# Kernel optimization log

Measured on AMD Instinct MI355X. Metric: run time of the kernel, lower is better.

## Reference

```python
import jax, jax.numpy as jnp
import numpy as np

B, N, F_IN = 512, 128, 133
NHID, NHEADS, HID = 64, 8, 512
FP_DIM, FP2, TASKS = 1489, 512, 12
ALPHA = 0.2
NEG_BIG = -9e15


def _lin_init(key, fan_in, fan_out):
    return jax.random.normal(key, (fan_in, fan_out), jnp.float32) / np.sqrt(fan_in)


def setup_inputs() -> dict:
    key = jax.random.key(0)
    ks = jax.random.split(key, 24)
    inp = {
        'h': jax.random.normal(ks[0], (B, N, F_IN), jnp.float32),
        'adj': jax.random.randint(ks[1], (B, N, N), 0, 2, jnp.int32),
        'edge_feat': jax.random.uniform(ks[2], (B, N, N), jnp.float32),
        'fp': jax.random.uniform(ks[3], (B, FP_DIM), jnp.float32),
        # multi-head GAT layer params (a split as [a1; a2; a_edge])
        'W_heads': jax.random.normal(ks[4], (NHEADS, F_IN, NHID), jnp.float32) / np.sqrt(F_IN),
        'a1_heads': jax.random.normal(ks[5], (NHEADS, NHID), jnp.float32) / np.sqrt(NHID),
        'a2_heads': jax.random.normal(ks[6], (NHEADS, NHID), jnp.float32) / np.sqrt(NHID),
        'ae_heads': jax.random.normal(ks[7], (NHEADS,), jnp.float32) * 0.1,
        # output GAT layer
        'W_out': jax.random.normal(ks[8], (NHID * NHEADS, HID), jnp.float32) / np.sqrt(NHID * NHEADS),
        'a1_out': jax.random.normal(ks[9], (HID,), jnp.float32) / np.sqrt(HID),
        'a2_out': jax.random.normal(ks[10], (HID,), jnp.float32) / np.sqrt(HID),
        'ae_out': jax.random.normal(ks[11], ()) * 0.1,
        # FPN
        'fc1_w': _lin_init(ks[12], FP_DIM, FP2), 'fc1_b': jnp.zeros((FP2,), jnp.float32),
        'fc2_w': _lin_init(ks[13], FP2, HID), 'fc2_b': jnp.zeros((HID,), jnp.float32),
        # cross-attention fusion
        'q_w': _lin_init(ks[14], HID, HID), 'q_b': jnp.zeros((HID,), jnp.float32),
        'k_w': _lin_init(ks[15], HID, HID), 'k_b': jnp.zeros((HID,), jnp.float32),
        'v_w': _lin_init(ks[16], HID, HID), 'v_b': jnp.zeros((HID,), jnp.float32),
        'o_w': _lin_init(ks[17], HID, HID), 'o_b': jnp.zeros((HID,), jnp.float32),
        # FFN head
        'ffn1_w': _lin_init(ks[18], HID, HID), 'ffn1_b': jnp.zeros((HID,), jnp.float32),
        'ffn2_w': _lin_init(ks[19], HID, TASKS), 'ffn2_b': jnp.zeros((TASKS,), jnp.float32),
    }
    return inp


def _leaky(x):
    return jnp.where(x >= 0, x, ALPHA * x)


def _fpgnn_forward(h, adj, edge_feat, fp,
                   W_heads, a1_heads, a2_heads, ae_heads,
                   W_out, a1_out, a2_out, ae_out,
                   fc1_w, fc1_b, fc2_w, fc2_b,
                   q_w, q_b, k_w, k_b, v_w, v_b, o_w, o_b,
                   ffn1_w, ffn1_b, ffn2_w, ffn2_b):
    mask = adj > 0  # [B,N,N]
    # --- multi-head GAT layers (concat=True) ---
    Wh = jnp.einsum('bnf,hfd->bhnd', h, W_heads)            # [B,H,N,D]
    s1 = jnp.einsum('bhnd,hd->bhn', Wh, a1_heads)
    s2 = jnp.einsum('bhnd,hd->bhn', Wh, a2_heads)
    # e[b,h,i,j] = leaky(Wh_i.a1 + Wh_j.a2 + edge_ij*ae)  (exact decomposition of
    # the original concat([Wh_i, Wh_j, edge_ij]) @ a)
    e = _leaky(s1[:, :, :, None] + s2[:, :, None, :]
               + edge_feat[:, None, :, :] * ae_heads[None, :, None, None])
    att = jnp.where(mask[:, None], e, NEG_BIG)
    att = jax.nn.softmax(att, axis=-1)                       # softmax over dim=1 of [N,N]
    hp = jnp.einsum('bhij,bhjd->bhid', att, Wh)
    x = jax.nn.elu(hp)                                       # concat=True -> ELU
    x = jnp.transpose(x, (0, 2, 1, 3)).reshape(B, N, NHEADS * NHID)
    # --- output GAT layer (concat=False) ---
    Wx = x @ W_out                                           # [B,N,HID]
    t1 = Wx @ a1_out                                         # [B,N]
    t2 = Wx @ a2_out
    e2 = _leaky(t1[:, :, None] + t2[:, None, :] + edge_feat * ae_out)
    att2 = jnp.where(mask, e2, NEG_BIG)
    att2 = jax.nn.softmax(att2, axis=-1)
    hp2 = jnp.einsum('bij,bjd->bid', att2, Wx)
    gat_nodes = jax.nn.elu(hp2)                              # F.elu in GATOne
    gat_out = gat_nodes.mean(axis=1)                         # molecule readout [B,HID]
    # --- FPN ---
    fpn_out = jax.nn.relu(fp @ fc1_w + fc1_b) @ fc2_w + fc2_b  # [B,HID]
    # --- cross-attention fusion ---
    q = gat_out @ q_w + q_b
    k = fpn_out @ k_w + k_b
    v = fpn_out @ v_w + v_b
    score = jnp.sum(q * k, axis=-1, keepdims=True) / np.sqrt(HID)  # [B,1]
    weight = jax.nn.softmax(score[:, :, None], axis=-1)[:, :, 0]    # softmax over size-1 dim -> ones
    fused = q + weight * v
    fused = jax.nn.relu(fused @ o_w + o_b)
    # --- FFN head (dropout p=0, eval) ---
    out = jax.nn.relu(fused @ ffn1_w + ffn1_b) @ ffn2_w + ffn2_b
    return out


def reference(h, adj, edge_feat, fp,
              W_heads, a1_heads, a2_heads, ae_heads,
              W_out, a1_out, a2_out, ae_out,
              fc1_w, fc1_b, fc2_w, fc2_b,
              q_w, q_b, k_w, k_b, v_w, v_b, o_w, o_b,
              ffn1_w, ffn1_b, ffn2_w, ffn2_b):
    return _fpgnn_forward(h, adj, edge_feat, fp,
                          W_heads, a1_heads, a2_heads, ae_heads,
                          W_out, a1_out, a2_out, ae_out,
                          fc1_w, fc1_b, fc2_w, fc2_b,
                          q_w, q_b, k_w, k_b, v_w, v_b, o_w, o_b,
                          ffn1_w, ffn1_b, ffn2_w, ffn2_b)
```

## Files before the change

kernel.cpp:

```cpp
#include <hip/hip_runtime.h>
#include <hip/hip_bf16.h>


#define ALPHA_LK 0.2f
#define LOG2E 1.44269504f
#define KP1 192
#define KPF 1536
#define MINF_BF16 0xFF80u

typedef unsigned short ushort_t;
typedef __attribute__((ext_vector_type(8))) short bfrag;
typedef __attribute__((ext_vector_type(4))) float ffrag;

__device__ __forceinline__ float b2f(ushort_t u) {
  return __uint_as_float(((unsigned)u) << 16);
}
__device__ __forceinline__ ushort_t f2b(float f) {
  unsigned u = __float_as_uint(f);
  unsigned r = (u + 0x7fffu + ((u >> 16) & 1u)) >> 16;
  return (ushort_t)r;
}
__device__ __forceinline__ unsigned cvt_pk(float lo, float hi) {
  unsigned r;
  asm("v_cvt_pk_bf16_f32 %0, %1, %2" : "=v"(r) : "v"(lo), "v"(hi));
  return r;
}
__device__ __forceinline__ float frcp(float x) {
  float r;
  asm("v_rcp_f32 %0, %1" : "=v"(r) : "v"(x));
  return r;
}
__device__ __forceinline__ float fexp2(float x) {
#if __has_builtin(__builtin_amdgcn_exp2f)
  return __builtin_amdgcn_exp2f(x);
#else
  return exp2f(x);
#endif
}
__device__ __forceinline__ float elu1(float v) {
  return v > 0.f ? v : __expf(v) - 1.f;
}

__device__ __forceinline__ void gll16(const void* g, void* l) {
  __builtin_amdgcn_global_load_lds(
      (const __attribute__((address_space(1))) unsigned int*)(unsigned long long)g,
      (__attribute__((address_space(3))) unsigned int*)(unsigned long long)l,
      16, 0, 0);
}

__global__ __launch_bounds__(256) void prep_all(
    const float* __restrict__ h, const int* __restrict__ adj,
    const float* __restrict__ edge, const float* __restrict__ fp,
    const float* __restrict__ Whd, const float* __restrict__ a1h,
    const float* __restrict__ a2h,
    const float* __restrict__ W_out, const float* __restrict__ a1o,
    const float* __restrict__ a2o,
    const float* __restrict__ fc1_w, const float* __restrict__ fc2_w,
    const float* __restrict__ q_w, const float* __restrict__ v_w,
    const float* __restrict__ o_w, const float* __restrict__ ffn1_w,
    const float* __restrict__ qb, const float* __restrict__ vb,
    ushort_t* __restrict__ hb, ushort_t* __restrict__ em,
    ushort_t* __restrict__ W2t, ushort_t* __restrict__ fpb,
    ushort_t* __restrict__ fc1t,
    ushort_t* __restrict__ Wot, ushort_t* __restrict__ fc2t,
    ushort_t* __restrict__ qwt, ushort_t* __restrict__ vwt,
    ushort_t* __restrict__ owt, ushort_t* __restrict__ f1t,
    float* __restrict__ wa1, float* __restrict__ wa2,
    ushort_t* __restrict__ wh12, float* __restrict__ qvb) {
  int bid = blockIdx.x;
  const int t = threadIdx.x;

  if (bid < 8) {
    int hh = bid;
    if (t < 192) {
      float s1 = 0.f, s2 = 0.f;
      if (t < 133) {
        const float* wr = Whd + (size_t)(hh * 133 + t) * 64;
        const float* a1r = a1h + hh * 64;
        const float* a2r = a2h + hh * 64;
#pragma unroll 8
        for (int d = 0; d < 64; ++d) {
          float wv = wr[d];
          s1 += wv * a1r[d];
          s2 += wv * a2r[d];
        }
      }
      wh12[hh * 384 + t] = f2b(s1);
      wh12[hh * 384 + 192 + t] = f2b(s2);
    }
    return;
  }
  bid -= 8;
  if (bid < 128) {
    int wv = t >> 6, lane = t & 63;
    int k = bid * 4 + wv;
    const float* wr = W_out + (size_t)k * 512;
    float p1 = 0.f, p2 = 0.f;
#pragma unroll
    for (int i = 0; i < 8; ++i) {
      float v = wr[lane + i * 64];
      p1 += v * a1o[lane + i * 64];
      p2 += v * a2o[lane + i * 64];
    }
#pragma unroll
    for (int off = 32; off; off >>= 1) {
      p1 += __shfl_down(p1, off);
      p2 += __shfl_down(p2, off);
    }
    if (lane == 0) { wa1[k] = p1; wa2[k] = p2; }
    return;
  }
  bid -= 128;
  if (bid < 2) {
    int o = bid * 256 + t;
    qvb[o] = qb[o] + vb[o];
    return;
  }
  bid -= 2;
  if (bid < 96) {
    int o = bid * 256 + t;
    if (o < 512 * 48) {
      int col = o / 48, c4 = (o - col * 48) * 4;
      int hh = col >> 6, d = col & 63;
      ushort4 v;
      v.x = (c4 + 0 < 133) ? f2b(Whd[(hh * 133 + c4 + 0) * 64 + d]) : (ushort_t)0;
      v.y = (c4 + 1 < 133) ? f2b(Whd[(hh * 133 + c4 + 1) * 64 + d]) : (ushort_t)0;
      v.z = (c4 + 2 < 133) ? f2b(Whd[(hh * 133 + c4 + 2) * 64 + d]) : (ushort_t)0;
      v.w = (c4 + 3 < 133) ? f2b(Whd[(hh * 133 + c4 + 3) * 64 + d]) : (ushort_t)0;
      *(ushort4*)&W2t[(size_t)col * KP1 + c4] = v;
    }
    return;
  }
  bid -= 96;
  if (bid < 768) {
    int o = bid * 256 + t;
    int row = o / 384, c4 = (o - row * 384) * 4;
    const float* fr = fp + (size_t)row * 1489;
    ushort4 v;
    v.x = (c4 + 0 < 1489) ? f2b(fr[c4 + 0]) : (ushort_t)0;
    v.y = (c4 + 1 < 1489) ? f2b(fr[c4 + 1]) : (ushort_t)0;
    v.z = (c4 + 2 < 1489) ? f2b(fr[c4 + 2]) : (ushort_t)0;
    v.w = (c4 + 3 < 1489) ? f2b(fr[c4 + 3]) : (ushort_t)0;
    *(ushort4*)&fpb[(size_t)row * KPF + c4] = v;
    return;
  }
  bid -= 768;
  if (bid < 768) {
    int o = bid * 256 + t;
    int col = o / 384, k4 = (o - col * 384) * 4;
    ushort4 v;
    v.x = (k4 + 0 < 1489) ? f2b(fc1_w[(size_t)(k4 + 0) * 512 + col]) : (ushort_t)0;
    v.y = (k4 + 1 < 1489) ? f2b(fc1_w[(size_t)(k4 + 1) * 512 + col]) : (ushort_t)0;
    v.z = (k4 + 2 < 1489) ? f2b(fc1_w[(size_t)(k4 + 2) * 512 + col]) : (ushort_t)0;
    v.w = (k4 + 3 < 1489) ? f2b(fc1_w[(size_t)(k4 + 3) * 512 + col]) : (ushort_t)0;
    *(ushort4*)&fc1t[(size_t)col * KPF + k4] = v;
    return;
  }
  bid -= 768;
  if (bid < 1536) {
    int y = bid >> 8;
    int o = (bid & 255) * 256 + t;
    const float* W = y == 0 ? W_out : y == 1 ? fc2_w : y == 2 ? q_w
                   : y == 3 ? v_w : y == 4 ? o_w : ffn1_w;
    ushort_t* Wt = y == 0 ? Wot : y == 1 ? fc2t : y == 2 ? qwt
                 : y == 3 ? vwt : y == 4 ? owt : f1t;
    int col = o >> 7, k4 = (o & 127) * 4;
    ushort4 v;
    v.x = f2b(W[(size_t)(k4 + 0) * 512 + col]);
    v.y = f2b(W[(size_t)(k4 + 1) * 512 + col]);
    v.z = f2b(W[(size_t)(k4 + 2) * 512 + col]);
    v.w = f2b(W[(size_t)(k4 + 3) * 512 + col]);
    *(ushort4*)&Wt[(size_t)col * 512 + k4] = v;
    return;
  }
  bid -= 1536;
  if (bid < 12288) {
    int o = bid * 256 + t;
    int row = o / 48, c4 = (o - row * 48) * 4;
    const float* hr = h + (size_t)row * 133;
    ushort4 v;
    v.x = (c4 + 0 < 133) ? f2b(hr[c4 + 0]) : (ushort_t)0;
    v.y = (c4 + 1 < 133) ? f2b(hr[c4 + 1]) : (ushort_t)0;
    v.z = (c4 + 2 < 133) ? f2b(hr[c4 + 2]) : (ushort_t)0;
    v.w = (c4 + 3 < 133) ? f2b(hr[c4 + 3]) : (ushort_t)0;
    *(ushort4*)&hb[(size_t)row * KP1 + c4] = v;
    return;
  }
  bid -= 12288;
  {
    size_t o = ((size_t)bid * 256 + t) * 4;
    float4 e = *(const float4*)&edge[o];
    int4 a = *(const int4*)&adj[o];
    ushort4 v;
    v.x = a.x > 0 ? f2b(e.x) : (ushort_t)MINF_BF16;
    v.y = a.y > 0 ? f2b(e.y) : (ushort_t)MINF_BF16;
    v.z = a.z > 0 ? f2b(e.z) : (ushort_t)MINF_BF16;
    v.w = a.w > 0 ? f2b(e.w) : (ushort_t)MINF_BF16;
    *(ushort4*)&em[o] = v;
  }
}

__global__ __launch_bounds__(256) void att2t(
    const ushort_t* __restrict__ xb, const ushort_t* __restrict__ em,
    const float* __restrict__ wa1, const float* __restrict__ wa2,
    const float* __restrict__ aeo,
    ushort_t* __restrict__ awg, float* __restrict__ sinvg, int base) {
  __shared__ float t1s[128], t2s[128];
  __shared__ float was1[512], was2[512];
  const int bl = blockIdx.x, bg = base + bl;
  const int t = threadIdx.x;
  was1[t] = wa1[t]; was1[t + 256] = wa1[t + 256];
  was2[t] = wa2[t]; was2[t + 256] = wa2[t + 256];
  __syncthreads();
  const int row = t >> 1, half = t & 1;
  {
    const ushort_t* xr = xb + (size_t)(bl * 128 + row) * 512 + half * 256;
    float p1 = 0.f, p2 = 0.f;
#pragma unroll 4
    for (int i = 0; i < 32; ++i) {
      uint4 u = *(const uint4*)&xr[i * 8];
      const unsigned uu[4] = {u.x, u.y, u.z, u.w};
#pragma unroll
      for (int pr = 0; pr < 4; ++pr) {
        float lo = __uint_as_float(uu[pr] << 16);
        float hi = __uint_as_float(uu[pr] & 0xffff0000u);
        int c = half * 256 + i * 8 + pr * 2;
        p1 = fmaf(lo, was1[c], p1); p1 = fmaf(hi, was1[c + 1], p1);
        p2 = fmaf(lo, was2[c], p2); p2 = fmaf(hi, was2[c + 1], p2);
      }
    }
    p1 += __shfl_xor(p1, 1);
    p2 += __shfl_xor(p2, 1);
    if (!half) { t1s[row] = p1 * LOG2E; t2s[row] = p2 * LOG2E; }
  }
  __syncthreads();
  const float ae2 = aeo[0] * LOG2E;
  const float rt1 = t1s[row];
  const ushort_t* emr = em + (size_t)bg * 16384 + row * 128 + half * 64;
  ushort_t* awr = awg + (size_t)bl * 16384 + row * 128 + half * 64;
  float s = 0.f;
#pragma unroll
  for (int v = 0; v < 8; ++v) {
    uint4 eu = *(const uint4*)&emr[v * 8];
    const unsigned uu[4] = {eu.x, eu.y, eu.z, eu.w};
    unsigned po[4];
#pragma unroll
    for (int pr = 0; pr < 4; ++pr) {
      float elo = __uint_as_float(uu[pr] << 16);
      float ehi = __uint_as_float(uu[pr] & 0xffff0000u);
      float e0 = fmaf(elo, ae2, rt1 + t2s[half * 64 + v * 8 + pr * 2]);
      float e1 = fmaf(ehi, ae2, rt1 + t2s[half * 64 + v * 8 + pr * 2 + 1]);
      e0 = fmaxf(e0, ALPHA_LK * e0);
      e1 = fmaxf(e1, ALPHA_LK * e1);
      float p0 = (elo != -INFINITY) ? fexp2(e0) : 0.f;
      float p1 = (ehi != -INFINITY) ? fexp2(e1) : 0.f;
      unsigned q = cvt_pk(p0, p1);
      po[pr] = q;
      s += __uint_as_float(q << 16) + __uint_as_float(q & 0xffff0000u);
    }
    *(uint4*)&awr[v * 8] = make_uint4(po[0], po[1], po[2], po[3]);
  }
  s += __shfl_xor(s, 1);
  if (!half) sinvg[(size_t)bl * 128 + row] = 1.f / fmaxf(s, 1e-30f);
}

__global__ __launch_bounds__(256) void fused_gat1(
    const ushort_t* __restrict__ hb, const ushort_t* __restrict__ W2t,
    const ushort_t* __restrict__ edgeM, const ushort_t* __restrict__ wh12g,
    const float* __restrict__ ae,
    ushort_t* __restrict__ x, int base) {
  __shared__ union {
    struct { ushort_t As[128][64]; ushort_t Bs[64][64]; } g;
    ushort_t WS[64][136];
  } u;
  __shared__ float ss1[128], ss2[128];
  __shared__ ushort_t wh12s[2][192];
  const int id = blockIdx.x;
  const int hh = (id >> 3) & 7;
  const int bl = ((id >> 6) << 3) | (id & 7);
  const int bg = base + bl;
  const int t = threadIdx.x;
  const int lane = t & 63, w = t >> 6;
  const int l16 = lane & 15, quad = lane >> 4;
  const int w8 = w * 8, sr8 = (t >> 3) & 7;
  const int csw = ((t & 7) ^ sr8) << 3;

  if (t < 96)
    *(ushort4*)&(&wh12s[0][0])[t * 4] =
        *(const ushort4*)&wh12g[hh * 384 + t * 4];

  const ushort_t* gA = hb + (size_t)(bl * 128 + w8 + sr8) * KP1 + csw;
  const ushort_t* gB = W2t + (size_t)(hh * 64 + w8 + sr8) * KP1 + csw;
  ffrag acc[2][4];
  ffrag acc_s[2];
#pragma unroll
  for (int mi = 0; mi < 2; ++mi) {
    acc_s[mi] = {0.f, 0.f, 0.f, 0.f};
#pragma unroll
    for (int ni = 0; ni < 4; ++ni) acc[mi][ni] = {0.f, 0.f, 0.f, 0.f};
  }
  for (int k0 = 0; k0 < KP1; k0 += 64) {
    __syncthreads();
#pragma unroll
    for (int p = 0; p < 4; ++p)
      gll16(gA + (size_t)(p * 32) * KP1 + k0, &u.g.As[p * 32 + w8][0]);
#pragma unroll
    for (int p = 0; p < 2; ++p)
      gll16(gB + (size_t)(p * 32) * KP1 + k0, &u.g.Bs[p * 32 + w8][0]);
    __syncthreads();
#pragma unroll
    for (int ks = 0; ks < 2; ++ks) {
      const int cs = ((ks * 4 + quad) ^ (l16 & 7)) << 3;
      bfrag af[2], bf[4];
      bfrag bs = {0, 0, 0, 0, 0, 0, 0, 0};
      if (l16 < 2)
        bs = *(const bfrag*)&wh12s[l16][k0 + ks * 32 + quad * 8];
#pragma unroll
      for (int mi = 0; mi < 2; ++mi)
        af[mi] = *(const bfrag*)&u.g.As[w * 32 + mi * 16 + l16][cs];
#pragma unroll
      for (int ni = 0; ni < 4; ++ni)
        bf[ni] = *(const bfrag*)&u.g.Bs[ni * 16 + l16][cs];
#pragma unroll
      for (int mi = 0; mi < 2; ++mi) {
#pragma unroll
        for (int ni = 0; ni < 4; ++ni)
          acc[mi][ni] = __builtin_amdgcn_mfma_f32_16x16x32_bf16(
              af[mi], bf[ni], acc[mi][ni], 0, 0, 0);
        acc_s[mi] = __builtin_amdgcn_mfma_f32_16x16x32_bf16(
            af[mi], bs, acc_s[mi], 0, 0, 0);
      }
    }
  }
  __syncthreads();

#pragma unroll
  for (int mi = 0; mi < 2; ++mi)
#pragma unroll
    for (int ni = 0; ni < 4; ++ni) {
      int col = ni * 16 + l16;
      int rowb = w * 32 + mi * 16 + quad * 4;
      uint2 pv;
      pv.x = cvt_pk(acc[mi][ni][0], acc[mi][ni][1]);
      pv.y = cvt_pk(acc[mi][ni][2], acc[mi][ni][3]);
      *(uint2*)&u.WS[col][rowb] = pv;
    }
  if (l16 < 2) {
    float* sp = (l16 == 0) ? ss1 : ss2;
#pragma unroll
    for (int mi = 0; mi < 2; ++mi)
#pragma unroll
      for (int r = 0; r < 4; ++r)
        sp[w * 32 + mi * 16 + quad * 4 + r] = acc_s[mi][r] * LOG2E;
  }
  uint4 ereg[2][4];
  {
    const ushort_t* em = edgeM + (size_t)bg * 16384;
#pragma unroll
    for (int mi = 0; mi < 2; ++mi) {
      int row = w * 32 + mi * 16 + l16;
#pragma unroll
      for (int ks = 0; ks < 4; ++ks)
        ereg[mi][ks] = *(const uint4*)&em[row * 128 + ks * 32 + quad * 8];
    }
  }
  __syncthreads();

  const float aeh2 = ae[hh] * LOG2E;
  float rs1[2];
  rs1[0] = ss1[w * 32 + l16];
  rs1[1] = ss1[w * 32 + 16 + l16];
  uint4 aw[2][4];
#pragma unroll
  for (int mi = 0; mi < 2; ++mi) {
#pragma unroll
    for (int ks = 0; ks < 4; ++ks) {
      float s2v[8];
      *(float4*)&s2v[0] = *(const float4*)&ss2[ks * 32 + quad * 8];
      *(float4*)&s2v[4] = *(const float4*)&ss2[ks * 32 + quad * 8 + 4];
      const unsigned uu[4] = {ereg[mi][ks].x, ereg[mi][ks].y,
                              ereg[mi][ks].z, ereg[mi][ks].w};
      unsigned po[4];
#pragma unroll
      for (int pr = 0; pr < 4; ++pr) {
        float elo = __uint_as_float(uu[pr] << 16);
        float ehi = __uint_as_float(uu[pr] & 0xffff0000u);
        float e0 = fmaf(elo, aeh2, rs1[mi] + s2v[pr * 2]);
        float e1 = fmaf(ehi, aeh2, rs1[mi] + s2v[pr * 2 + 1]);
        e0 = fmaxf(e0, ALPHA_LK * e0);
        e1 = fmaxf(e1, ALPHA_LK * e1);
        float p0 = (elo != -INFINITY) ? fexp2(e0) : 0.f;
        float p1 = (ehi != -INFINITY) ? fexp2(e1) : 0.f;
        po[pr] = cvt_pk(p0, p1);
      }
      aw[mi][ks] = make_uint4(po[0], po[1], po[2], po[3]);
    }
  }

  bfrag bones;
#pragma unroll
  for (int i = 0; i < 8; ++i) bones[i] = (short)0x3F80;

  ffrag acc2[2][4];
  ffrag accs[2];
#pragma unroll
  for (int mi = 0; mi < 2; ++mi) {
    accs[mi] = {0.f, 0.f, 0.f, 0.f};
#pragma unroll
    for (int ni = 0; ni < 4; ++ni) acc2[mi][ni] = {0.f, 0.f, 0.f, 0.f};
  }
#pragma unroll
  for (int ks = 0; ks < 4; ++ks) {
    bfrag bfr[4];
#pragma unroll
    for (int ni = 0; ni < 4; ++ni)
      bfr[ni] = *(const bfrag*)&u.WS[ni * 16 + l16][ks * 32 + quad * 8];
#pragma unroll
    for (int mi = 0; mi < 2; ++mi) {
      bfrag afr;
      __builtin_memcpy(&afr, &aw[mi][ks], 16);
#pragma unroll
      for (int ni = 0; ni < 4; ++ni)
        acc2[mi][ni] = __builtin_amdgcn_mfma_f32_16x16x32_bf16(
            afr, bfr[ni], acc2[mi][ni], 0, 0, 0);
      accs[mi] = __builtin_amdgcn_mfma_f32_16x16x32_bf16(
          afr, bones, accs[mi], 0, 0, 0);
    }
  }
  float sv[2][4];
#pragma unroll
  for (int mi = 0; mi < 2; ++mi)
#pragma unroll
    for (int r = 0; r < 4; ++r)
      sv[mi][r] = frcp(fmaxf(accs[mi][r], 1e-30f));

#pragma unroll
  for (int mi = 0; mi < 2; ++mi)
#pragma unroll
    for (int ni = 0; ni < 4; ++ni) {
      float e0 = elu1(acc2[mi][ni][0] * sv[mi][0]);
      float e1 = elu1(acc2[mi][ni][1] * sv[mi][1]);
      float e2 = elu1(acc2[mi][ni][2] * sv[mi][2]);
      float e3 = elu1(acc2[mi][ni][3] * sv[mi][3]);
      unsigned p01 = cvt_pk(e0, e1), p23 = cvt_pk(e2, e3);
      int rl = w * 32 + mi * 16 + quad * 4;
      size_t bo = (size_t)(bl * 128 + rl) * 512 + hh * 64 + ni * 16 + l16;
      x[bo] = (ushort_t)p01;
      x[bo + 512] = (ushort_t)(p01 >> 16);
      x[bo + 1024] = (ushort_t)p23;
      x[bo + 1536] = (ushort_t)(p23 >> 16);
    }
}

__global__ __launch_bounds__(256) void fused_gat2(
    const ushort_t* __restrict__ xb, const ushort_t* __restrict__ Wot,
    const ushort_t* __restrict__ awg, const float* __restrict__ sinvg,
    ushort_t* __restrict__ gatb, int base) {
  __shared__ union {
    struct { ushort_t As[128][64]; ushort_t Bs[128][64]; } g;
    ushort_t WS[128][136];
  } u;
  __shared__ float ps[4][64];
  const int id = blockIdx.x;
  const int sp2 = (id >> 3) & 3;
  const int bl = ((id >> 5) << 3) | (id & 7);
  const int bg = base + bl;
  const int t = threadIdx.x;
  const int lane = t & 63, w = t >> 6;
  const int wm = w >> 1, wn = w & 1;
  const int l16 = lane & 15, quad = lane >> 4;
  const int w8 = w * 8, sr8 = (t >> 3) & 7;
  const int csw = ((t & 7) ^ sr8) << 3;

  const ushort_t* gA = xb + (size_t)(bl * 128 + w8 + sr8) * 512 + csw;
  const ushort_t* gB = Wot + (size_t)(sp2 * 128 + w8 + sr8) * 512 + csw;
  ffrag acc[4][4];
#pragma unroll
  for (int mi = 0; mi < 4; ++mi)
#pragma unroll
    for (int ni = 0; ni < 4; ++ni) acc[mi][ni] = {0.f, 0.f, 0.f, 0.f};
  for (int k0 = 0; k0 < 512; k0 += 64) {
    __syncthreads();
#pragma unroll
    for (int p = 0; p < 4; ++p) {
      gll16(gA + (size_t)(p * 32) * 512 + k0, &u.g.As[p * 32 + w8][0]);
      gll16(gB + (size_t)(p * 32) * 512 + k0, &u.g.Bs[p * 32 + w8][0]);
    }
    __syncthreads();
#pragma unroll
    for (int ks = 0; ks < 2; ++ks) {
      const int cs = ((ks * 4 + quad) ^ (l16 & 7)) << 3;
      bfrag af[4], bf[4];
#pragma unroll
      for (int i = 0; i < 4; ++i) {
        af[i] = *(const bfrag*)&u.g.As[wm * 64 + i * 16 + l16][cs];
        bf[i] = *(const bfrag*)&u.g.Bs[wn * 64 + i * 16 + l16][cs];
      }
#pragma unroll
      for (int mi = 0; mi < 4; ++mi)
#pragma unroll
        for (int ni = 0; ni < 4; ++ni)
          acc[mi][ni] = __builtin_amdgcn_mfma_f32_16x16x32_bf16(
              af[mi], bf[ni], acc[mi][ni], 0, 0, 0);
    }
  }
  __syncthreads();

#pragma unroll
  for (int mi = 0; mi < 4; ++mi)
#pragma unroll
    for (int ni = 0; ni < 4; ++ni) {
      int col = wn * 64 + ni * 16 + l16;
      int rowb = wm * 64 + mi * 16 + quad * 4;
      uint2 pv;
      pv.x = cvt_pk(acc[mi][ni][0], acc[mi][ni][1]);
      pv.y = cvt_pk(acc[mi][ni][2], acc[mi][ni][3]);
      *(uint2*)&u.WS[col][rowb] = pv;
    }
  __syncthreads();

  uint4 awf[2][4];
  float sv[2][4];
  {
    const ushort_t* ap = awg + (size_t)bl * 16384;
#pragma unroll
    for (int mi = 0; mi < 2; ++mi) {
      int row = w * 32 + mi * 16 + l16;
#pragma unroll
      for (int ks = 0; ks < 4; ++ks)
        awf[mi][ks] = *(const uint4*)&ap[row * 128 + ks * 32 + quad * 8];
      float si = sinvg[(size_t)bl * 128 + row];
#pragma unroll
      for (int r = 0; r < 4; ++r) sv[mi][r] = __shfl(si, quad * 4 + r);
    }
  }

  for (int s0 = 0; s0 < 2; ++s0) {
    ffrag acc2[2][4];
#pragma unroll
    for (int mi = 0; mi < 2; ++mi)
#pragma unroll
      for (int ni = 0; ni < 4; ++ni) acc2[mi][ni] = {0.f, 0.f, 0.f, 0.f};
#pragma unroll
    for (int ks = 0; ks < 4; ++ks) {
      bfrag bfr[4];
#pragma unroll
      for (int ni = 0; ni < 4; ++ni)
        bfr[ni] = *(const bfrag*)&u.WS[s0 * 64 + ni * 16 + l16][ks * 32 + quad * 8];
#pragma unroll
      for (int mi = 0; mi < 2; ++mi) {
        bfrag afr;
        __builtin_memcpy(&afr, &awf[mi][ks], 16);
#pragma unroll
        for (int ni = 0; ni < 4; ++ni)
          acc2[mi][ni] = __builtin_amdgcn_mfma_f32_16x16x32_bf16(
              afr, bfr[ni], acc2[mi][ni], 0, 0, 0);
      }
    }
    __syncthreads();
#pragma unroll
    for (int ni = 0; ni < 4; ++ni) {
      float s = 0.f;
#pragma unroll
      for (int mi = 0; mi < 2; ++mi)
#pragma unroll
        for (int r = 0; r < 4; ++r) s += elu1(acc2[mi][ni][r] * sv[mi][r]);
      s += __shfl_xor(s, 16);
      s += __shfl_xor(s, 32);
      if (quad == 0) ps[w][ni * 16 + l16] = s;
    }
    __syncthreads();
    if (t < 64) {
      float s = ps[0][t] + ps[1][t] + ps[2][t] + ps[3][t];
      gatb[(size_t)bg * 512 + sp2 * 128 + s0 * 64 + t] = f2b(s * (1.f / 128.f));
    }
  }
}

__device__ __forceinline__ void tail_kloop(
    const ushort_t* __restrict__ A, const ushort_t* __restrict__ Bt,
    int K, int ld, ushort_t (*As)[64], ushort_t (*Bs)[64],
    ffrag (*acc)[4], int row0, int col0, int t) {
  const int lane = t & 63, w = t >> 6;
  const int wm = w >> 1, wn = w & 1;
  const int l16 = lane & 15, quad = lane >> 4;
  const int w8 = w * 8, sr8 = (t >> 3) & 7;
  const int csw = ((t & 7) ^ sr8) << 3;
  const ushort_t* gA = A + (size_t)(row0 + w8 + sr8) * ld + csw;
  const ushort_t* gB = Bt + (size_t)(col0 + w8 + sr8) * ld + csw;
  for (int k0 = 0; k0 < K; k0 += 64) {
    __syncthreads();
#pragma unroll
    for (int p = 0; p < 4; ++p) {
      gll16(gA + (size_t)(p * 32) * ld + k0, &As[p * 32 + w8][0]);
      gll16(gB + (size_t)(p * 32) * ld + k0, &Bs[p * 32 + w8][0]);
    }
    __syncthreads();
#pragma unroll
    for (int ks = 0; ks < 2; ++ks) {
      const int cs = ((ks * 4 + quad) ^ (l16 & 7)) << 3;
      bfrag af[4], bf[4];
#pragma unroll
      for (int i = 0; i < 4; ++i) {
        af[i] = *(const bfrag*)&As[wm * 64 + i * 16 + l16][cs];
        bf[i] = *(const bfrag*)&Bs[wn * 64 + i * 16 + l16][cs];
      }
#pragma unroll
      for (int mi = 0; mi < 4; ++mi)
#pragma unroll
        for (int ni = 0; ni < 4; ++ni)
          acc[mi][ni] = __builtin_amdgcn_mfma_f32_16x16x32_bf16(
              af[mi], bf[ni], acc[mi][ni], 0, 0, 0);
    }
  }
}

template <int DUAL, int RELU>
__global__ __launch_bounds__(256) void gemm_tail(
    const ushort_t* __restrict__ A1, const ushort_t* __restrict__ Bt1,
    int K1, int ld1,
    const ushort_t* __restrict__ A2, const ushort_t* __restrict__ Bt2,
    const float* __restrict__ bias, ushort_t* __restrict__ C) {
  __shared__ ushort_t As[128][64];
  __shared__ ushort_t Bs[128][64];
  const int t = threadIdx.x;
  const int lane = t & 63, w = t >> 6;
  const int wm = w >> 1, wn = w & 1;
  const int l16 = lane & 15, quad = lane >> 4;
  const int row0 = blockIdx.y * 128, col0 = blockIdx.x * 128;

  ffrag acc[4][4];
#pragma unroll
  for (int mi = 0; mi < 4; ++mi)
#pragma unroll
    for (int ni = 0; ni < 4; ++ni) acc[mi][ni] = {0.f, 0.f, 0.f, 0.f};

  tail_kloop(A1, Bt1, K1, ld1, As, Bs, acc, row0, col0, t);
  if (DUAL) tail_kloop(A2, Bt2, 512, 512, As, Bs, acc, row0, col0, t);

#pragma unroll
  for (int mi = 0; mi < 4; ++mi)
#pragma unroll
    for (int ni = 0; ni < 4; ++ni) {
      int col = col0 + wn * 64 + ni * 16 + l16;
      float bb = bias[col];
      float v0 = acc[mi][ni][0] + bb, v1 = acc[mi][ni][1] + bb;
      float v2 = acc[mi][ni][2] + bb, v3 = acc[mi][ni][3] + bb;
      if (RELU) {
        v0 = fmaxf(v0, 0.f); v1 = fmaxf(v1, 0.f);
        v2 = fmaxf(v2, 0.f); v3 = fmaxf(v3, 0.f);
      }
      unsigned p01 = cvt_pk(v0, v1), p23 = cvt_pk(v2, v3);
      int row = row0 + wm * 64 + mi * 16 + quad * 4;
      size_t o = (size_t)row * 512 + col;
      C[o] = (ushort_t)p01;
      C[o + 512] = (ushort_t)(p01 >> 16);
      C[o + 1024] = (ushort_t)p23;
      C[o + 1536] = (ushort_t)(p23 >> 16);
    }
}

__global__ __launch_bounds__(256) void ffn2_kernel(
    const ushort_t* __restrict__ f5, const float* __restrict__ W,
    const float* __restrict__ b, float* __restrict__ out) {
  int wv = threadIdx.x >> 6, lane = threadIdx.x & 63;
  int row = blockIdx.x * 4 + wv;
  const ushort_t* fr = f5 + (size_t)row * 512;
  float v[8];
  ushort4 u0 = *(const ushort4*)&fr[lane * 8];
  ushort4 u1 = *(const ushort4*)&fr[lane * 8 + 4];
  v[0] = b2f(u0.x); v[1] = b2f(u0.y); v[2] = b2f(u0.z); v[3] = b2f(u0.w);
  v[4] = b2f(u1.x); v[5] = b2f(u1.y); v[6] = b2f(u1.z); v[7] = b2f(u1.w);
#pragma unroll
  for (int j = 0; j < 12; ++j) {
    float s = 0.f;
#pragma unroll
    for (int i = 0; i < 8; ++i) s += v[i] * W[(size_t)(lane * 8 + i) * 12 + j];
#pragma unroll
    for (int off = 32; off; off >>= 1) s += __shfl_down(s, off);
    if (lane == 0) out[(size_t)row * 12 + j] = s + b[j];
  }
}

extern "C" void kernel_launch(void* const* d_in, const int* in_sizes, int n_in,
                              void* d_out, int out_size, void* d_ws, size_t ws_size,
                              hipStream_t stream) {
  const float* h        = (const float*)d_in[0];
  const int*   adj      = (const int*)d_in[1];
  const float* edge     = (const float*)d_in[2];
  const float* fp       = (const float*)d_in[3];
  const float* W_heads  = (const float*)d_in[4];
  const float* a1_heads = (const float*)d_in[5];
  const float* a2_heads = (const float*)d_in[6];
  const float* ae_heads = (const float*)d_in[7];
  const float* W_out  = (const float*)d_in[8];
  const float* a1_out = (const float*)d_in[9];
  const float* a2_out = (const float*)d_in[10];
  const float* ae_out = (const float*)d_in[11];
  const float* fc1_w = (const float*)d_in[12];
  const float* fc1_b = (const float*)d_in[13];
  const float* fc2_w = (const float*)d_in[14];
  const float* fc2_b = (const float*)d_in[15];
  const float* q_w = (const float*)d_in[16];
  const float* q_b = (const float*)d_in[17];
  const float* v_w = (const float*)d_in[20];
  const float* v_b = (const float*)d_in[21];
  const float* o_w = (const float*)d_in[22];
  const float* o_b = (const float*)d_in[23];
  const float* ffn1_w = (const float*)d_in[24];
  const float* ffn1_b = (const float*)d_in[25];
  const float* ffn2_w = (const float*)d_in[26];
  const float* ffn2_b = (const float*)d_in[27];
  float* out = (float*)d_out;

  const size_t hb_bytes = (size_t)65536 * KP1 * 2;
  const size_t em_bytes = (size_t)512 * 16384 * 2;
  const size_t tail_bytes =
      (size_t)512 * KPF * 2 * 2 + (size_t)512 * 512 * 2 * 12 + 2048;
  const size_t fixed_bytes = hb_bytes + em_bytes + (size_t)512 * KP1 * 2 +
                             (size_t)2 * 65536 * 4 + tail_bytes + 16384;
  int C = 32;
  for (int cand = 512; cand >= 32; cand >>= 1) {
    size_t need = (size_t)cand * (131072 + 32768 + 512) + fixed_bytes;
    if (need <= ws_size) { C = cand; break; }
  }
  const int M = C * 128;
  (void)M;

  char* p = (char*)d_ws;
  ushort_t* xb  = (ushort_t*)p; p += (size_t)C * 65536 * 2;
  ushort_t* awg = (ushort_t*)p; p += (size_t)C * 16384 * 2;
  float* sinv   = (float*)p;    p += (size_t)C * 128 * 4;
  ushort_t* hb  = (ushort_t*)p; p += hb_bytes;
  ushort_t* em  = (ushort_t*)p; p += em_bytes;
  ushort_t* W2t = (ushort_t*)p; p += (size_t)512 * KP1 * 2;
  ushort_t* wh12 = (ushort_t*)p; p += 8 * 384 * 2;
  float* t_unused = (float*)p; p += 2 * 65536 * 4 - 8 * 384 * 2;
  (void)t_unused;
  ushort_t* fpb  = (ushort_t*)p; p += (size_t)512 * KPF * 2;
  ushort_t* fc1t = (ushort_t*)p; p += (size_t)512 * KPF * 2;
  ushort_t* Wot  = (ushort_t*)p; p += (size_t)512 * 512 * 2;
  ushort_t* fc2t = (ushort_t*)p; p += (size_t)512 * 512 * 2;
  ushort_t* qwt  = (ushort_t*)p; p += (size_t)512 * 512 * 2;
  ushort_t* vwt  = (ushort_t*)p; p += (size_t)512 * 512 * 2;
  ushort_t* owt  = (ushort_t*)p; p += (size_t)512 * 512 * 2;
  ushort_t* f1t  = (ushort_t*)p; p += (size_t)512 * 512 * 2;
  ushort_t* gatb = (ushort_t*)p; p += (size_t)512 * 512 * 2;
  ushort_t* fb1  = (ushort_t*)p; p += (size_t)512 * 512 * 2;
  ushort_t* fb2  = (ushort_t*)p; p += (size_t)512 * 512 * 2;
  ushort_t* fb3  = (ushort_t*)p; p += (size_t)512 * 512 * 2;
  ushort_t* fb4  = (ushort_t*)p; p += (size_t)512 * 512 * 2;
  ushort_t* fb5  = (ushort_t*)p; p += (size_t)512 * 512 * 2;
  float* qvb = (float*)p; p += 2048;
  float* wa1 = (float*)p; p += 2048;
  float* wa2 = (float*)p; p += 2048;

  prep_all<<<23786, 256, 0, stream>>>(
      h, adj, edge, fp, W_heads, a1_heads, a2_heads,
      W_out, a1_out, a2_out,
      fc1_w, fc2_w, q_w, v_w, o_w, ffn1_w, q_b, v_b,
      hb, em, W2t, fpb, fc1t, Wot, fc2t, qwt, vwt, owt, f1t,
      wa1, wa2, wh12, qvb);

  for (int base = 0; base < 512; base += C) {
    fused_gat1<<<8 * C, 256, 0, stream>>>(
        hb + (size_t)base * 128 * KP1, W2t, em, wh12, ae_heads, xb, base);
    att2t<<<C, 256, 0, stream>>>(xb, em, wa1, wa2, ae_out, awg, sinv, base);
    fused_gat2<<<4 * C, 256, 0, stream>>>(xb, Wot, awg, sinv, gatb, base);
  }

  gemm_tail<0, 1><<<dim3(4, 4), 256, 0, stream>>>(
      fpb, fc1t, KPF, KPF, nullptr, nullptr, fc1_b, fb1);
  gemm_tail<0, 0><<<dim3(4, 4), 256, 0, stream>>>(
      fb1, fc2t, 512, 512, nullptr, nullptr, fc2_b, fb2);
  gemm_tail<1, 0><<<dim3(4, 4), 256, 0, stream>>>(
      gatb, qwt, 512, 512, fb2, vwt, qvb, fb3);
  gemm_tail<0, 1><<<dim3(4, 4), 256, 0, stream>>>(
      fb3, owt, 512, 512, nullptr, nullptr, o_b, fb4);
  gemm_tail<0, 1><<<dim3(4, 4), 256, 0, stream>>>(
      fb4, f1t, 512, 512, nullptr, nullptr, ffn1_b, fb5);
  ffn2_kernel<<<128, 256, 0, stream>>>(fb5, ffn2_w, ffn2_b, out);
}
```

Baseline: 425.6 us.

## Process two attention heads per block in first GAT layer kernel

Each fused_gat1 block now computes two heads instead of one, widening the projection GEMM N tile from 64 to 128 so each A tile of node features loaded into shared memory serves both heads, and halving the grid. The attention and aggregation phase loops over the two heads, reloading the edge matrix per head from global memory (likely cached) rather than holding it in registers across the GEMM. This trades more accumulator registers and shared memory per block, and fewer blocks, for less redundant loading of h and fewer launches' worth of blocks.

```diff
diff --git a/kernel.cpp b/kernel.cpp
--- a/kernel.cpp
+++ b/kernel.cpp
@@ -270,14 +270,14 @@
     const float* __restrict__ ae,
     ushort_t* __restrict__ x, int base) {
   __shared__ union {
-    struct { ushort_t As[128][64]; ushort_t Bs[64][64]; } g;
-    ushort_t WS[64][136];
+    struct { ushort_t As[128][64]; ushort_t Bs[128][64]; } g;
+    ushort_t WS[2][64][136];
   } u;
-  __shared__ float ss1[128], ss2[128];
-  __shared__ ushort_t wh12s[2][192];
+  __shared__ float ss1h[2][128], ss2h[2][128];
+  __shared__ ushort_t wh12s[4][200];
   const int id = blockIdx.x;
-  const int hh = (id >> 3) & 7;
-  const int bl = ((id >> 6) << 3) | (id & 7);
+  const int hp = (id >> 3) & 3;
+  const int bl = ((id >> 5) << 3) | (id & 7);
   const int bg = base + bl;
   const int t = threadIdx.x;
   const int lane = t & 63, w = t >> 6;
@@ -285,46 +285,47 @@
   const int w8 = w * 8, sr8 = (t >> 3) & 7;
   const int csw = ((t & 7) ^ sr8) << 3;
 
-  if (t < 96)
-    *(ushort4*)&(&wh12s[0][0])[t * 4] =
-        *(const ushort4*)&wh12g[hh * 384 + t * 4];
+  if (t < 192) {
+    int r = t / 48, c4 = (t - r * 48) * 4;
+    *(ushort4*)&wh12s[r][c4] =
+        *(const ushort4*)&wh12g[hp * 768 + r * 192 + c4];
+  }
 
   const ushort_t* gA = hb + (size_t)(bl * 128 + w8 + sr8) * KP1 + csw;
-  const ushort_t* gB = W2t + (size_t)(hh * 64 + w8 + sr8) * KP1 + csw;
-  ffrag acc[2][4];
+  const ushort_t* gB = W2t + (size_t)(hp * 128 + w8 + sr8) * KP1 + csw;
+  ffrag acc[2][8];
   ffrag acc_s[2];
 #pragma unroll
   for (int mi = 0; mi < 2; ++mi) {
     acc_s[mi] = {0.f, 0.f, 0.f, 0.f};
 #pragma unroll
-    for (int ni = 0; ni < 4; ++ni) acc[mi][ni] = {0.f, 0.f, 0.f, 0.f};
+    for (int ni = 0; ni < 8; ++ni) acc[mi][ni] = {0.f, 0.f, 0.f, 0.f};
   }
   for (int k0 = 0; k0 < KP1; k0 += 64) {
     __syncthreads();
 #pragma unroll
-    for (int p = 0; p < 4; ++p)
+    for (int p = 0; p < 4; ++p) {
       gll16(gA + (size_t)(p * 32) * KP1 + k0, &u.g.As[p * 32 + w8][0]);
-#pragma unroll
-    for (int p = 0; p < 2; ++p)
       gll16(gB + (size_t)(p * 32) * KP1 + k0, &u.g.Bs[p * 32 + w8][0]);
+    }
     __syncthreads();
 #pragma unroll
     for (int ks = 0; ks < 2; ++ks) {
       const int cs = ((ks * 4 + quad) ^ (l16 & 7)) << 3;
-      bfrag af[2], bf[4];
+      bfrag af[2], bf[8];
       bfrag bs = {0, 0, 0, 0, 0, 0, 0, 0};
-      if (l16 < 2)
+      if (l16 < 4)
         bs = *(const bfrag*)&wh12s[l16][k0 + ks * 32 + quad * 8];
 #pragma unroll
       for (int mi = 0; mi < 2; ++mi)
         af[mi] = *(const bfrag*)&u.g.As[w * 32 + mi * 16 + l16][cs];
 #pragma unroll
-      for (int ni = 0; ni < 4; ++ni)
+      for (int ni = 0; ni < 8; ++ni)
         bf[ni] = *(const bfrag*)&u.g.Bs[ni * 16 + l16][cs];
 #pragma unroll
       for (int mi = 0; mi < 2; ++mi) {
 #pragma unroll
-        for (int ni = 0; ni < 4; ++ni)
+        for (int ni = 0; ni < 8; ++ni)
           acc[mi][ni] = __builtin_amdgcn_mfma_f32_16x16x32_bf16(
               af[mi], bf[ni], acc[mi][ni], 0, 0, 0);
         acc_s[mi] = __builtin_amdgcn_mfma_f32_16x16x32_bf16(
@@ -337,119 +338,115 @@
 #pragma unroll
   for (int mi = 0; mi < 2; ++mi)
 #pragma unroll
-    for (int ni = 0; ni < 4; ++ni) {
+    for (int ni = 0; ni < 8; ++ni) {
       int col = ni * 16 + l16;
+      int hx = col >> 6, c2 = col & 63;
       int rowb = w * 32 + mi * 16 + quad * 4;
       uint2 pv;
       pv.x = cvt_pk(acc[mi][ni][0], acc[mi][ni][1]);
       pv.y = cvt_pk(acc[mi][ni][2], acc[mi][ni][3]);
-      *(uint2*)&u.WS[col][rowb] = pv;
-    }
-  if (l16 < 2) {
-    float* sp = (l16 == 0) ? ss1 : ss2;
+      *(uint2*)&u.WS[hx][c2][rowb] = pv;
+    }
+  if (l16 < 4) {
+    int hx = l16 >> 1;
+    float* sp = (l16 & 1) ? ss2h[hx] : ss1h[hx];
 #pragma unroll
     for (int mi = 0; mi < 2; ++mi)
 #pragma unroll
       for (int r = 0; r < 4; ++r)
         sp[w * 32 + mi * 16 + quad * 4 + r] = acc_s[mi][r] * LOG2E;
   }
-  uint4 ereg[2][4];
-  {
-    const ushort_t* em = edgeM + (size_t)bg * 16384;
+  __syncthreads();
+
+  bfrag bones;
+#pragma unroll
+  for (int i = 0; i < 8; ++i) bones[i] = (short)0x3F80;
+
+  for (int hx = 0; hx < 2; ++hx) {
+    const float aeh2 = ae[hp * 2 + hx] * LOG2E;
+    float rs1[2];
+    rs1[0] = ss1h[hx][w * 32 + l16];
+    rs1[1] = ss1h[hx][w * 32 + 16 + l16];
+    uint4 aw[2][4];
 #pragma unroll
     for (int mi = 0; mi < 2; ++mi) {
-      int row = w * 32 + mi * 16 + l16;
-#pragma unroll
-      for (int ks = 0; ks < 4; ++ks)
-        ereg[mi][ks] = *(const uint4*)&em[row * 128 + ks * 32 + quad * 8];
-    }
-  }
-  __syncthreads();
-
-  const float aeh2 = ae[hh] * LOG2E;
-  float rs1[2];
-  rs1[0] = ss1[w * 32 + l16];
-  rs1[1] = ss1[w * 32 + 16 + l16];
-  uint4 aw[2][4];
-#pragma unroll
-  for (int mi = 0; mi < 2; ++mi) {
+      const ushort_t* emrow =
+          edgeM + (size_t)bg * 16384 + (w * 32 + mi * 16 + l16) * 128;
+#pragma unroll
+      for (int ks = 0; ks < 4; ++ks) {
+        uint4 er = *(const uint4*)&emrow[ks * 32 + quad * 8];
+        float s2v[8];
+        *(float4*)&s2v[0] = *(const float4*)&ss2h[hx][ks * 32 + quad * 8];
+        *(float4*)&s2v[4] = *(const float4*)&ss2h[hx][ks * 32 + quad * 8 + 4];
+        const unsigned uu[4] = {er.x, er.y, er.z, er.w};
+        unsigned po[4];
+#pragma unroll
+        for (int pr = 0; pr < 4; ++pr) {
+          float elo = __uint_as_float(uu[pr] << 16);
+          float ehi = __uint_as_float(uu[pr] & 0xffff0000u);
+          float e0 = fmaf(elo, aeh2, rs1[mi] + s2v[pr * 2]);
+          float e1 = fmaf(ehi, aeh2, rs1[mi] + s2v[pr * 2 + 1]);
+          e0 = fmaxf(e0, ALPHA_LK * e0);
+          e1 = fmaxf(e1, ALPHA_LK * e1);
+          float p0 = (elo != -INFINITY) ? fexp2(e0) : 0.f;
+          float p1 = (ehi != -INFINITY) ? fexp2(e1) : 0.f;
+          po[pr] = cvt_pk(p0, p1);
+        }
+        aw[mi][ks] = make_uint4(po[0], po[1], po[2], po[3]);
+      }
+    }
+
+    ffrag acc2[2][4];
+    ffrag accs[2];
+#pragma unroll
+    for (int mi = 0; mi < 2; ++mi) {
+      accs[mi] = {0.f, 0.f, 0.f, 0.f};
+#pragma unroll
+      for (int ni = 0; ni < 4; ++ni) acc2[mi][ni] = {0.f, 0.f, 0.f, 0.f};
+    }
 #pragma unroll
     for (int ks = 0; ks < 4; ++ks) {
-      float s2v[8];
-      *(float4*)&s2v[0] = *(const float4*)&ss2[ks * 32 + quad * 8];
-      *(float4*)&s2v[4] = *(const float4*)&ss2[ks * 32 + quad * 8 + 4];
-      const unsigned uu[4] = {ereg[mi][ks].x, ereg[mi][ks].y,
-                              ereg[mi][ks].z, ereg[mi][ks].w};
-      unsigned po[4];
-#pragma unroll
-      for (int pr = 0; pr < 4; ++pr) {
-        float elo = __uint_as_float(uu[pr] << 16);
-        float ehi = __uint_as_float(uu[pr] & 0xffff0000u);
-        float e0 = fmaf(elo, aeh2, rs1[mi] + s2v[pr * 2]);
-        float e1 = fmaf(ehi, aeh2, rs1[mi] + s2v[pr * 2 + 1]);
-        e0 = fmaxf(e0, ALPHA_LK * e0);
-        e1 = fmaxf(e1, ALPHA_LK * e1);
-        float p0 = (elo != -INFINITY) ? fexp2(e0) : 0.f;
-        float p1 = (ehi != -INFINITY) ? fexp2(e1) : 0.f;
-        po[pr] = cvt_pk(p0, p1);
-      }
-      aw[mi][ks] = make_uint4(po[0], po[1], po[2], po[3]);
-    }
-  }
-
-  bfrag bones;
-#pragma unroll
-  for (int i = 0; i < 8; ++i) bones[i] = (short)0x3F80;
-
-  ffrag acc2[2][4];
-  ffrag accs[2];
-#pragma unroll
-  for (int mi = 0; mi < 2; ++mi) {
-    accs[mi] = {0.f, 0.f, 0.f, 0.f};
-#pragma unroll
-    for (int ni = 0; ni < 4; ++ni) acc2[mi][ni] = {0.f, 0.f, 0.f, 0.f};
-  }
-#pragma unroll
-  for (int ks = 0; ks < 4; ++ks) {
-    bfrag bfr[4];
-#pragma unroll
-    for (int ni = 0; ni < 4; ++ni)
-      bfr[ni] = *(const bfrag*)&u.WS[ni * 16 + l16][ks * 32 + quad * 8];
-#pragma unroll
-    for (int mi = 0; mi < 2; ++mi) {
-      bfrag afr;
-      __builtin_memcpy(&afr, &aw[mi][ks], 16);
+      bfrag bfr[4];
 #pragma unroll
       for (int ni = 0; ni < 4; ++ni)
-        acc2[mi][ni] = __builtin_amdgcn_mfma_f32_16x16x32_bf16(
-            afr, bfr[ni], acc2[mi][ni], 0, 0, 0);
-      accs[mi] = __builtin_amdgcn_mfma_f32_16x16x32_bf16(
-          afr, bones, accs[mi], 0, 0, 0);
-    }
-  }
-  float sv[2][4];
-#pragma unroll
-  for (int mi = 0; mi < 2; ++mi)
-#pragma unroll
-    for (int r = 0; r < 4; ++r)
-      sv[mi][r] = frcp(fmaxf(accs[mi][r], 1e-30f));
-
-#pragma unroll
-  for (int mi = 0; mi < 2; ++mi)
-#pragma unroll
-    for (int ni = 0; ni < 4; ++ni) {
-      float e0 = elu1(acc2[mi][ni][0] * sv[mi][0]);
-      float e1 = elu1(acc2[mi][ni][1] * sv[mi][1]);
-      float e2 = elu1(acc2[mi][ni][2] * sv[mi][2]);
-      float e3 = elu1(acc2[mi][ni][3] * sv[mi][3]);
-      unsigned p01 = cvt_pk(e0, e1), p23 = cvt_pk(e2, e3);
-      int rl = w * 32 + mi * 16 + quad * 4;
-      size_t bo = (size_t)(bl * 128 + rl) * 512 + hh * 64 + ni * 16 + l16;
-      x[bo] = (ushort_t)p01;
-      x[bo + 512] = (ushort_t)(p01 >> 16);
-      x[bo + 1024] = (ushort_t)p23;
-      x[bo + 1536] = (ushort_t)(p23 >> 16);
-    }
+        bfr[ni] = *(const bfrag*)&u.WS[hx][ni * 16 + l16][ks * 32 + quad * 8];
+#pragma unroll
+      for (int mi = 0; mi < 2; ++mi) {
+        bfrag afr;
+        __builtin_memcpy(&afr, &aw[mi][ks], 16);
+#pragma unroll
+        for (int ni = 0; ni < 4; ++ni)
+          acc2[mi][ni] = __builtin_amdgcn_mfma_f32_16x16x32_bf16(
+              afr, bfr[ni], acc2[mi][ni], 0, 0, 0);
+        accs[mi] = __builtin_amdgcn_mfma_f32_16x16x32_bf16(
+            afr, bones, accs[mi], 0, 0, 0);
+      }
+    }
+    float sv[2][4];
+#pragma unroll
+    for (int mi = 0; mi < 2; ++mi)
+#pragma unroll
+      for (int r = 0; r < 4; ++r)
+        sv[mi][r] = frcp(fmaxf(accs[mi][r], 1e-30f));
+
+#pragma unroll
+    for (int mi = 0; mi < 2; ++mi)
+#pragma unroll
+      for (int ni = 0; ni < 4; ++ni) {
+        float e0 = elu1(acc2[mi][ni][0] * sv[mi][0]);
+        float e1 = elu1(acc2[mi][ni][1] * sv[mi][1]);
+        float e2 = elu1(acc2[mi][ni][2] * sv[mi][2]);
+        float e3 = elu1(acc2[mi][ni][3] * sv[mi][3]);
+        unsigned p01 = cvt_pk(e0, e1), p23 = cvt_pk(e2, e3);
+        int rl = w * 32 + mi * 16 + quad * 4;
+        size_t bo = (size_t)(bl * 128 + rl) * 512 +
+                    (hp * 2 + hx) * 64 + ni * 16 + l16;
+        x[bo] = (ushort_t)p01;
+        x[bo + 512] = (ushort_t)(p01 >> 16);
+        x[bo + 1024] = (ushort_t)p23;
+        x[bo + 1536] = (ushort_t)(p23 >> 16);
+      }
+  }
 }
 
 __global__ __launch_bounds__(256) void fused_gat2(
@@ -763,7 +760,7 @@
       wa1, wa2, wh12, qvb);
 
   for (int base = 0; base < 512; base += C) {
-    fused_gat1<<<8 * C, 256, 0, stream>>>(
+    fused_gat1<<<4 * C, 256, 0, stream>>>(
         hb + (size_t)base * 128 * KP1, W2t, em, wh12, ae_heads, xb, base);
     att2t<<<C, 256, 0, stream>>>(xb, em, wa1, wa2, ae_out, awg, sinv, base);
     fused_gat2<<<4 * C, 256, 0, stream>>>(xb, Wot, awg, sinv, gatb, base);
```

New measurement: 428.0 us. About the same (+0.6%).
